# Optimization experiments

Measured on AMD Instinct MI355X. Metric: run time of the kernel, lower is better.

## Reference

```python
import jax, jax.numpy as jnp
import numpy as np

K, P = 20, 20  # neighbors and progressive enlargement step


def _conv1x1(w, x):  # w: (Cout, Cin), x: (B, Cin, N) -> (B, Cout, N)
    return jnp.einsum('oc,bcn->bon', w, x)


def _group_norm(x, gamma, beta, groups, eps=1e-5):  # x: (B, C, N)
    B, C, N = x.shape
    xg = x.reshape(B, groups, C // groups, N)
    m = jnp.mean(xg, axis=(2, 3), keepdims=True)
    v = jnp.var(xg, axis=(2, 3), keepdims=True)
    xn = ((xg - m) * jax.lax.rsqrt(v + eps)).reshape(B, C, N)
    return xn * gamma[None, :, None] + beta[None, :, None]


def _block(x, w, g, b, groups):  # Conv1d(k=1) + GroupNorm + LeakyReLU(0.2)
    h = _group_norm(_conv1x1(w, x), g, b, groups)
    return jnp.where(h > 0, h, 0.2 * h)


def _gather_max(f, idx):  # f: (B, C, N), idx: (B, N, k) -> (B, C, N)
    ft = jnp.swapaxes(f, 1, 2)  # (B, N, C)
    g = jax.vmap(lambda ff, ii: ff[ii])(ft, idx)  # (B, N, k, C)
    return jnp.swapaxes(jnp.max(g, axis=2), 1, 2)


def _forward(x,
             w1a, g1a, b1a, w1b, g1b, b1b,
             w2a, g2a, b2a, w2b, g2b, b2b,
             w3a, g3a, b3a, w3b, g3b, b3b,
             w4a, g4a, b4a, w4b, g4b, b4b,
             w5_1, g5_1, b5_1, w5_2, g5_2, b5_2):
    xc = jnp.swapaxes(x, 1, 2)  # (B, C, N)
    # knn_acc: negative squared pairwise distance, take top-(k+3P)
    xx = jnp.sum(xc * xc, axis=1, keepdims=True)  # (B, 1, N)
    inner = jnp.einsum('bcn,bcm->bnm', xc, xc)  # (B, N, N)
    pd = 2.0 * inner - jnp.swapaxes(xx, 1, 2) - xx  # -||xi-xj||^2
    _, idx_pool = jax.lax.top_k(pd, K + 3 * P)  # (B, N, k+3P)

    def layer(xin, wa, ga, ba, wb, gb, bb, groups, idx):
        fa = _block(xin, wa, ga, ba, groups)
        fb = _block(xin, wb, gb, bb, groups)
        return _gather_max(fa, idx) + fb

    x1 = layer(xc, w1a, g1a, b1a, w1b, g1b, b1b, 8, idx_pool[:, :, :K])
    x2 = layer(x1, w2a, g2a, b2a, w2b, g2b, b2b, 8, idx_pool[:, :, :K + P])
    x3 = layer(x2, w3a, g3a, b3a, w3b, g3b, b3b, 8, idx_pool[:, :, :K + 2 * P])
    x4 = layer(x3, w4a, g4a, b4a, w4b, g4b, b4b, 16, idx_pool)
    x_cat = jnp.concatenate([x1, x2, x3, x4], axis=1)  # (B, 512, N)
    h = _block(x_cat, w5_1, g5_1, b5_1, 16)  # (B, 1024, N)
    h = _block(h, w5_2, g5_2, b5_2, 16)      # (B, 512, N)
    return jnp.swapaxes(h, 1, 2)  # (B, N, 512)


def setup_inputs() -> dict:
    key = jax.random.key(0)
    ks = iter(jax.random.split(key, 16))
    d = {"x": jax.random.normal(next(ks), (8, 2048, 3), dtype=jnp.float32)}

    def add(name, cout, cin):
        d["w" + name] = jax.random.normal(next(ks), (cout, cin), dtype=jnp.float32) * 0.1
        d["g" + name] = jnp.ones((cout,), dtype=jnp.float32)
        d["b" + name] = jnp.zeros((cout,), dtype=jnp.float32)

    add("1a", 64, 3); add("1b", 64, 3)
    add("2a", 64, 64); add("2b", 64, 64)
    add("3a", 128, 64); add("3b", 128, 64)
    add("4a", 256, 128); add("4b", 256, 128)
    add("5_1", 1024, 512); add("5_2", 512, 1024)
    return d


def reference(x,
              w1a, g1a, b1a, w1b, g1b, b1b,
              w2a, g2a, b2a, w2b, g2b, b2b,
              w3a, g3a, b3a, w3b, g3b, b3b,
              w4a, g4a, b4a, w4b, g4b, b4b,
              w5_1, g5_1, b5_1, w5_2, g5_2, b5_2):
    return _forward(x,
                    w1a, g1a, b1a, w1b, g1b, b1b,
                    w2a, g2a, b2a, w2b, g2b, b2b,
                    w3a, g3a, b3a, w3b, g3b, b3b,
                    w4a, g4a, b4a, w4b, g4b, b4b,
                    w5_1, g5_1, b5_1, w5_2, g5_2, b5_2)
```

## Files before the change

kernel.cpp:

```cpp
#include <hip/hip_runtime.h>
#include <stdint.h>

typedef unsigned short u16;
typedef unsigned int u32;
typedef unsigned long long u64;
typedef __attribute__((ext_vector_type(8))) __bf16 bf16x8;
typedef __attribute__((ext_vector_type(8))) u16 u16x8;
typedef __attribute__((ext_vector_type(4))) float f32x4;

#define DEVI __device__ __forceinline__

DEVI u16 f2bf(float f) {
  u32 u = __float_as_uint(f);
  u += 0x7FFFu + ((u >> 16) & 1u);
  return (u16)(u >> 16);
}
DEVI float bf2f(u16 h) { return __uint_as_float(((u32)h) << 16); }
DEVI u16 mono(u16 b) {
  return (b & 0x8000u) ? (u16)~b : (u16)(b | 0x8000u);
}
DEVI u16 unmono(u16 t) {
  return (t & 0x8000u) ? (u16)(t ^ 0x8000u) : (u16)(~t);
}

DEVI void glds16(const void* g, void* l) {
  __builtin_amdgcn_global_load_lds((const __attribute__((address_space(1))) void*)g,
                                   (__attribute__((address_space(3))) void*)l, 16, 0, 0);
}

__global__ void k_pack_all(const float* __restrict__ x, float4* __restrict__ c4,
                           float* __restrict__ gsum,
                           const float* __restrict__ w2a, const float* __restrict__ w2b,
                           const float* __restrict__ w3a, const float* __restrict__ w3b,
                           const float* __restrict__ w4a, const float* __restrict__ w4b,
                           const float* __restrict__ w51, const float* __restrict__ w52,
                           u16* __restrict__ wbf) {
  int g = blockIdx.x * 256 + threadIdx.x;
  if (g < 1792) gsum[g] = 0.f;
  if (g < 16384) {
    float x0 = x[g*3], x1 = x[g*3+1], x2 = x[g*3+2];
    float n = __fadd_rn(__fadd_rn(__fmul_rn(x0,x0), __fmul_rn(x1,x1)), __fmul_rn(x2,x2));
    c4[g] = make_float4(x0, x1, x2, n);
  }
  const float* s; int off;
  if      (g <    4096) { s = w2a; off = g; }
  else if (g <    8192) { s = w2b; off = g - 4096; }
  else if (g <   16384) { s = w3a; off = g - 8192; }
  else if (g <   24576) { s = w3b; off = g - 16384; }
  else if (g <   57344) { s = w4a; off = g - 24576; }
  else if (g <   90112) { s = w4b; off = g - 57344; }
  else if (g <  614400) { s = w51; off = g - 90112; }
  else                  { s = w52; off = g - 614400; }
  wbf[g] = f2bf(s[off]);
}

__global__ __launch_bounds__(256, 8) void k_knn(const float4* __restrict__ c4, int* __restrict__ idxp) {
  __shared__ u64 cand[4][128];
  const int wid = threadIdx.x >> 6;
  const int lane = threadIdx.x & 63;
  const int batch = blockIdx.x & 7;
  const int qib = (blockIdx.x >> 3) * 4 + wid;
  const int blk = (batch << 11) + qib;
  const float4* cb = c4 + (batch << 11);
  const float4 q = cb[qib];

  u32 key[32];
  #pragma unroll
  for (int s = 0; s < 32; ++s) {
    float4 c = cb[s*64 + lane];
    float inner = __fadd_rn(__fadd_rn(__fmul_rn(q.x,c.x), __fmul_rn(q.y,c.y)), __fmul_rn(q.z,c.z));
    float pd = __fsub_rn(__fsub_rn(__fmul_rn(2.0f, inner), q.w), c.w);
    u32 bits = __float_as_uint(pd);
    key[s] = (bits & 0x80000000u) ? ~bits : (bits | 0x80000000u);
  }

  u32 T = 0;
  for (int bit = 30; bit >= 0; --bit) {
    u32 Tc = T | (1u << bit);
    int c = 0;
    #pragma unroll
    for (int s = 0; s < 32; ++s)
      c += __popcll(__ballot(key[s] >= Tc));
    if (c >= 80) { T = Tc; if (c <= 128) break; }
  }

  cand[wid][lane] = 0ull;
  cand[wid][lane + 64] = 0ull;
  asm volatile("s_waitcnt lgkmcnt(0)" ::: "memory");

  const u64 below = (lane == 0) ? 0ull : (~0ull >> (64 - lane));
  int base = 0;
  #pragma unroll
  for (int s = 0; s < 32; ++s) {
    u64 msk = __ballot(key[s] >= T);
    if (key[s] >= T) {
      int pos = base + (int)__popcll(msk & below);
      if (pos < 128)
        cand[wid][pos] = (((u64)key[s]) << 32) | (u32)(2047 - (s*64 + lane));
    }
    base += (int)__popcll(msk);
  }
  asm volatile("s_waitcnt lgkmcnt(0)" ::: "memory");

  u64 v0 = cand[wid][lane];
  u64 v1 = cand[wid][lane + 64];
  #pragma unroll
  for (int k2 = 2; k2 <= 128; k2 <<= 1) {
    #pragma unroll
    for (int j = k2 >> 1; j > 0; j >>= 1) {
      if (j == 64) {
        u64 mx = v0 > v1 ? v0 : v1;
        u64 mn = v0 > v1 ? v1 : v0;
        v0 = mx; v1 = mn;
      } else {
        u64 p0 = __shfl_xor(v0, j, 64);
        u64 p1 = __shfl_xor(v1, j, 64);
        bool lowlane = ((lane & j) == 0);
        bool d0 = ((lane & k2) == 0);
        bool d1 = (((lane + 64) & k2) == 0);
        bool wm0 = (d0 == lowlane);
        bool wm1 = (d1 == lowlane);
        u64 mx0 = v0 > p0 ? v0 : p0, mn0 = v0 > p0 ? p0 : v0;
        u64 mx1 = v1 > p1 ? v1 : p1, mn1 = v1 > p1 ? p1 : v1;
        v0 = wm0 ? mx0 : mn0;
        v1 = wm1 ? mx1 : mn1;
      }
    }
  }

  idxp[(size_t)blk*80 + lane] = 2047 - (int)(u32)v0;
  if (lane < 16) idxp[(size_t)blk*80 + 64 + lane] = 2047 - (int)(u32)v1;
}

__global__ __launch_bounds__(256) void k_conv1(const float* __restrict__ x,
    const float* __restrict__ w1a, const float* __restrict__ w1b,
    const float* __restrict__ g1a, const float* __restrict__ g1b,
    u16* __restrict__ out, float* __restrict__ gsum) {
  __shared__ float xs[384];
  __shared__ float colsum[128], colss[128];
  const int tid = threadIdx.x;
  const int P0 = blockIdx.x * 128;
  for (int i = tid; i < 384; i += 256) xs[i] = x[P0*3 + i];
  if (tid < 128) { colsum[tid] = 0.f; colss[tid] = 0.f; }
  __syncthreads();

  const int c = tid & 127;
  const int half = tid >> 7;
  const float* w = (c < 64) ? (w1a + 3*c) : (w1b + 3*(c-64));
  float wx = w[0], wy = w[1], wz = w[2];
  float gam = (c < 64) ? g1a[c] : g1b[c-64];
  u16 flip = (gam < 0.f) ? (u16)0xFFFF : (u16)0;

  float s = 0.f, ss = 0.f;
  #pragma unroll 4
  for (int p_ = 0; p_ < 64; ++p_) {
    int p = (half << 6) + p_;
    float h = wx*xs[p*3] + wy*xs[p*3+1] + wz*xs[p*3+2];
    s += h; ss += h*h;
    out[(size_t)(P0 + p)*128 + c] = (u16)(mono(f2bf(h)) ^ flip);
  }
  atomicAdd(&colsum[c], s);
  atomicAdd(&colss[c], ss);
  __syncthreads();
  if (tid < 16) {
    float gs = 0.f, gss = 0.f;
    #pragma unroll
    for (int q = 0; q < 8; ++q) { gs += colsum[tid*8+q]; gss += colss[tid*8+q]; }
    int b = blockIdx.x >> 4;
    atomicAdd(&gsum[(b*16 + tid)*2],   gs);
    atomicAdd(&gsum[(b*16 + tid)*2+1], gss);
  }
}

__global__ __launch_bounds__(256) void k_gather(const u16* __restrict__ conv, int Ctot, int Ca,
    int CgShift, int NG, const float* __restrict__ gsum,
    const float* __restrict__ ga, const float* __restrict__ ba,
    const float* __restrict__ gb, const float* __restrict__ bb,
    const int* __restrict__ idxp, int k,
    u16* __restrict__ xcat, int outOff, int lppShift) {
  const int batch = blockIdx.x & 7;
  const int blkin = blockIdx.x >> 3;
  const int lgid = blkin * 256 + threadIdx.x;
  const int p_in = lgid >> lppShift;
  const int c8 = (lgid & ((1 << lppShift) - 1)) * 8;
  const int p = (batch << 11) + p_in;
  const int* irow = idxp + (size_t)p * 80;
  const u16* cb = conv + ((size_t)(batch << 11)) * Ctot + c8;

  const int gia = c8 >> CgShift;
  const int gib = (Ca + c8) >> CgShift;
  const float cnt = (float)(2048 << CgShift);
  float2 sa = *(const float2*)(gsum + (size_t)(batch*NG + gia)*2);
  float2 sb = *(const float2*)(gsum + (size_t)(batch*NG + gib)*2);
  float meanA = sa.x / cnt, rstdA = rsqrtf(sa.y / cnt - meanA*meanA + 1e-5f);
  float meanB = sb.x / cnt, rstdB = rsqrtf(sb.y / cnt - meanB*meanB + 1e-5f);

  float gav[8], bav[8], gbv[8], bbv[8];
  *(float4*)&gav[0] = *(const float4*)(ga + c8); *(float4*)&gav[4] = *(const float4*)(ga + c8 + 4);
  *(float4*)&bav[0] = *(const float4*)(ba + c8); *(float4*)&bav[4] = *(const float4*)(ba + c8 + 4);
  *(float4*)&gbv[0] = *(const float4*)(gb + c8); *(float4*)&gbv[4] = *(const float4*)(gb + c8 + 4);
  *(float4*)&bbv[0] = *(const float4*)(bb + c8); *(float4*)&bbv[4] = *(const float4*)(bb + c8 + 4);

  u16x8 fbv = *(const u16x8*)(conv + (size_t)p * Ctot + Ca + c8);

  u16x8 m8 = (u16x8)(u16)0;
  for (int j0 = 0; j0 < k; j0 += 4) {
    int4 mi4 = *(const int4*)(irow + j0);
    int mis[4] = {mi4.x, mi4.y, mi4.z, mi4.w};
    u16x8 rows[4];
    #pragma unroll
    for (int u = 0; u < 4; ++u)
      rows[u] = *(const u16x8*)(cb + (size_t)mis[u] * Ctot);
    #pragma unroll
    for (int u = 0; u < 4; ++u)
      m8 = __builtin_elementwise_max(m8, rows[u]);
  }

  u16 ov[8];
  #pragma unroll
  for (int q = 0; q < 8; ++q) {
    u16 fA = (gav[q] < 0.f) ? (u16)0xFFFF : (u16)0;
    u16 fB = (gbv[q] < 0.f) ? (u16)0xFFFF : (u16)0;
    float xa = bf2f(unmono((u16)((u16)m8[q] ^ fA)));
    float ha = (xa - meanA) * rstdA * gav[q] + bav[q];
    ha = ha > 0.f ? ha : 0.2f * ha;
    float xb = bf2f(unmono((u16)((u16)fbv[q] ^ fB)));
    float hb = (xb - meanB) * rstdB * gbv[q] + bbv[q];
    hb = hb > 0.f ? hb : 0.2f * hb;
    ov[q] = f2bf(ha + hb);
  }
  *(u16x8*)(xcat + (size_t)p * 512 + outOff + c8) = *(u16x8*)ov;
}

__global__ void k_sb51(const float* __restrict__ gsum, const float* __restrict__ g,
                       const float* __restrict__ b, float* __restrict__ sc,
                       float* __restrict__ bi) {
  int i = blockIdx.x * 256 + threadIdx.x;
  int bb = i >> 10, c = i & 1023;
  int grp = c >> 6;
  float2 s = *(const float2*)(gsum + (size_t)(bb*16 + grp)*2);
  float mean = s.x / 131072.f;
  float rstd = rsqrtf(s.y / 131072.f - mean*mean + 1e-5f);
  float A = rstd * g[c];
  sc[i] = A;
  bi[i] = b[c] - mean * A;
}

__global__ __launch_bounds__(256) void k_apply52(const u16* __restrict__ h2,
    float* __restrict__ outp, const float* __restrict__ gsum,
    const float* __restrict__ g, const float* __restrict__ b) {
  int gid = blockIdx.x * 256 + threadIdx.x;
  size_t e = (size_t)gid * 8;
  int row = (int)(e >> 9);
  int c = (int)e & 511;
  int grp = c >> 5;
  float2 s = *(const float2*)(gsum + (size_t)((row >> 11)*16 + grp)*2);
  const float cnt = 65536.f;
  float mean = s.x / cnt, rstd = rsqrtf(s.y / cnt - mean*mean + 1e-5f);
  u16x8 v = *(const u16x8*)(h2 + e);
  float gv[8], bv[8];
  *(float4*)&gv[0] = *(const float4*)(g + c); *(float4*)&gv[4] = *(const float4*)(g + c + 4);
  *(float4*)&bv[0] = *(const float4*)(b + c); *(float4*)&bv[4] = *(const float4*)(b + c + 4);
  float h[8];
  #pragma unroll
  for (int q = 0; q < 8; ++q) {
    float xv = bf2f((u16)v[q]);
    float o = (xv - mean) * rstd * gv[q] + bv[q];
    h[q] = o > 0.f ? o : 0.2f * o;
  }
  *(float4*)(outp + e)     = make_float4(h[0], h[1], h[2], h[3]);
  *(float4*)(outp + e + 4) = make_float4(h[4], h[5], h[6], h[7]);
}

template<int OUTF32, int MONO, int TRANSA>
__global__ __launch_bounds__(256) void k_gemm(const u16* __restrict__ A, int lda,
    const u16* __restrict__ Bw, int K, void* __restrict__ outp, int ldc,
    int CgShift, int NG, float* __restrict__ gsum,
    const float* __restrict__ ga, const float* __restrict__ gb, int Ca,
    const float* __restrict__ scA, const float* __restrict__ biA) {
  constexpr int BK = 64;
  __shared__ __align__(16) u16 As[128 * BK];
  __shared__ __align__(16) u16 Bs[128 * BK];
  __shared__ float colsum[128], colss[128];
  const int tid = threadIdx.x;
  const int wid = tid >> 6, lane = tid & 63;
  const int tileM = blockIdx.x * 128, tileN = blockIdx.y * 128;
  const int wm = wid >> 1, wn = wid & 1;
  const int lr = lane & 15, lk = (lane >> 4) * 8;
  const float* scb = TRANSA ? (scA + (size_t)(tileM >> 11) * 1024) : nullptr;
  const float* bib = TRANSA ? (biA + (size_t)(tileM >> 11) * 1024) : nullptr;
  f32x4 acc[4][4] = {};
  for (int k0 = 0; k0 < K; k0 += BK) {
    __syncthreads();
    #pragma unroll
    for (int i = 0; i < 4; ++i) {
      int flat = i * 256 + tid;
      int row = flat >> 3, ck = flat & 7;
      if (TRANSA) {
        int cbase = k0 + ck * 8;
        uint4 v = *(const uint4*)(A + (size_t)(tileM + row) * lda + cbase);
        float4 s0 = *(const float4*)(scb + cbase);
        float4 s1 = *(const float4*)(scb + cbase + 4);
        float4 b0 = *(const float4*)(bib + cbase);
        float4 b1 = *(const float4*)(bib + cbase + 4);
        float sc8[8] = {s0.x,s0.y,s0.z,s0.w,s1.x,s1.y,s1.z,s1.w};
        float bi8[8] = {b0.x,b0.y,b0.z,b0.w,b1.x,b1.y,b1.z,b1.w};
        u32 vv[4] = {v.x, v.y, v.z, v.w};
        u32 ov[4];
        #pragma unroll
        for (int q2 = 0; q2 < 4; ++q2) {
          float x0 = bf2f((u16)(vv[q2] & 0xFFFF));
          float x1 = bf2f((u16)(vv[q2] >> 16));
          float o0 = x0 * sc8[q2*2]   + bi8[q2*2];
          float o1 = x1 * sc8[q2*2+1] + bi8[q2*2+1];
          o0 = o0 > 0.f ? o0 : 0.2f * o0;
          o1 = o1 > 0.f ? o1 : 0.2f * o1;
          ov[q2] = (u32)f2bf(o0) | (((u32)f2bf(o1)) << 16);
        }
        *(uint4*)((char*)As + flat * 16) = make_uint4(ov[0], ov[1], ov[2], ov[3]);
      } else {
        glds16(A + (size_t)(tileM + row) * lda + (k0 + ck * 8), (char*)As + flat * 16);
      }
    }
    #pragma unroll
    for (int i = 0; i < 4; ++i) {
      int flat = i * 256 + tid;
      int row = flat >> 3, ck = flat & 7;
      glds16(Bw + (size_t)(tileN + row) * K + (k0 + ck * 8), (char*)Bs + flat * 16);
    }
    __syncthreads();
    #pragma unroll
    for (int ks = 0; ks < 2; ++ks) {
      bf16x8 af[4], bfr[4];
      #pragma unroll
      for (int i = 0; i < 4; ++i)
        af[i] = *(const bf16x8*)&As[(wm*64 + i*16 + lr) * BK + ks*32 + lk];
      #pragma unroll
      for (int j = 0; j < 4; ++j)
        bfr[j] = *(const bf16x8*)&Bs[(wn*64 + j*16 + lr) * BK + ks*32 + lk];
      #pragma unroll
      for (int i = 0; i < 4; ++i)
        #pragma unroll
        for (int j = 0; j < 4; ++j)
          acc[i][j] = __builtin_amdgcn_mfma_f32_16x16x32_bf16(af[i], bfr[j], acc[i][j], 0, 0, 0);
    }
  }
  const int orow0 = tileM + wm*64 + ((lane >> 4) * 4);
  const int ocol0 = tileN + wn*64 + lr;

  u16 flip[4] = {0,0,0,0};
  if (MONO) {
    #pragma unroll
    for (int j = 0; j < 4; ++j) {
      int colg = ocol0 + j*16;
      float gm = (colg < Ca) ? ga[colg] : gb[colg - Ca];
      flip[j] = (gm < 0.f) ? (u16)0xFFFF : (u16)0;
    }
  }

  float csum[4] = {0.f,0.f,0.f,0.f}, css[4] = {0.f,0.f,0.f,0.f};
  #pragma unroll
  for (int i = 0; i < 4; ++i)
    #pragma unroll
    for (int j = 0; j < 4; ++j)
      #pragma unroll
      for (int r = 0; r < 4; ++r) {
        int row = orow0 + i*16 + r;
        int col = ocol0 + j*16;
        float v = acc[i][j][r];
        csum[j] += v; css[j] += v*v;
        if (OUTF32) ((float*)outp)[(size_t)row * ldc + col] = v;
        else {
          u16 st = f2bf(v);
          if (MONO) st = (u16)(mono(st) ^ flip[j]);
          ((u16*)outp)[(size_t)row * ldc + col] = st;
        }
      }

  #pragma unroll
  for (int mask = 16; mask <= 32; mask <<= 1)
    #pragma unroll
    for (int j = 0; j < 4; ++j) {
      csum[j] += __shfl_xor(csum[j], mask, 64);
      css[j]  += __shfl_xor(css[j],  mask, 64);
    }
  if (tid < 128) { colsum[tid] = 0.f; colss[tid] = 0.f; }
  __syncthreads();
  if ((lane >> 4) == 0) {
    #pragma unroll
    for (int j = 0; j < 4; ++j) {
      int col = wn*64 + j*16 + lr;
      atomicAdd(&colsum[col], csum[j]);
      atomicAdd(&colss[col],  css[j]);
    }
  }
  __syncthreads();
  const int NGtile = 128 >> CgShift;
  if (tid < NGtile) {
    float s = 0.f, ss = 0.f;
    const int Cg = 1 << CgShift;
    for (int c0 = tid << CgShift; c0 < (tid << CgShift) + Cg; ++c0) { s += colsum[c0]; ss += colss[c0]; }
    int b = tileM >> 11;
    int gidx = (tileN >> CgShift) + tid;
    atomicAdd(&gsum[(size_t)(b*NG + gidx)*2],   s);
    atomicAdd(&gsum[(size_t)(b*NG + gidx)*2+1], ss);
  }
}

extern "C" void kernel_launch(void* const* d_in, const int* in_sizes, int n_in,
                              void* d_out, int out_size, void* d_ws, size_t ws_size,
                              hipStream_t stream) {
  const float* x   = (const float*)d_in[0];
  const float* w1a = (const float*)d_in[1];
  const float* g1a = (const float*)d_in[2];
  const float* b1a = (const float*)d_in[3];
  const float* w1b = (const float*)d_in[4];
  const float* g1b = (const float*)d_in[5];
  const float* b1b = (const float*)d_in[6];
  const float* w2a = (const float*)d_in[7];
  const float* g2a = (const float*)d_in[8];
  const float* b2a = (const float*)d_in[9];
  const float* w2b = (const float*)d_in[10];
  const float* g2b = (const float*)d_in[11];
  const float* b2b = (const float*)d_in[12];
  const float* w3a = (const float*)d_in[13];
  const float* g3a = (const float*)d_in[14];
  const float* b3a = (const float*)d_in[15];
  const float* w3b = (const float*)d_in[16];
  const float* g3b = (const float*)d_in[17];
  const float* b3b = (const float*)d_in[18];
  const float* w4a = (const float*)d_in[19];
  const float* g4a = (const float*)d_in[20];
  const float* b4a = (const float*)d_in[21];
  const float* w4b = (const float*)d_in[22];
  const float* g4b = (const float*)d_in[23];
  const float* b4b = (const float*)d_in[24];
  const float* w51 = (const float*)d_in[25];
  const float* g51 = (const float*)d_in[26];
  const float* b51 = (const float*)d_in[27];
  const float* w52 = (const float*)d_in[28];
  const float* g52 = (const float*)d_in[29];
  const float* b52 = (const float*)d_in[30];

  char* ws = (char*)d_ws;
  int*    idxp   = (int*)   (ws + 0);
  float4* c4     = (float4*)(ws + 5242880);
  u16*    wbf    = (u16*)   (ws + 5505024);
  float*  gsum   = (float*) (ws + 7782400);
  u16*    convAB = (u16*)   (ws + 7790592);
  u16*    h1     = (u16*)   (ws + 24567808);
  u16*    xcat   = (u16*)   (ws + 58122240);
  float*  sc51   = (float*) (ws + 0);
  float*  bi51   = (float*) (ws + 32768);
  u16*    h2     = (u16*)   (ws + 7790592);
  u16* wc2 = wbf, *wc3 = wbf + 8192, *wc4 = wbf + 24576;
  u16* w51b = wbf + 90112, *w52b = wbf + 614400;
  float* outf = (float*)d_out;
  float* gsL1 = gsum;        float* gsL2 = gsum + 256;  float* gsL3 = gsum + 512;
  float* gsL4 = gsum + 768;  float* gs51 = gsum + 1280; float* gs52 = gsum + 1536;

  k_pack_all<<<4448, 256, 0, stream>>>(x, c4, gsum, w2a, w2b, w3a, w3b, w4a, w4b,
                                       w51, w52, wbf);
  k_knn<<<4096, 256, 0, stream>>>(c4, idxp);

  k_conv1<<<128, 256, 0, stream>>>(x, w1a, w1b, g1a, g1b, convAB, gsL1);
  k_gather<<<512, 256, 0, stream>>>(convAB, 128, 64, 3, 16, gsL1,
                                    g1a, b1a, g1b, b1b, idxp, 20, xcat, 0, 3);

  k_gemm<0,1,0><<<dim3(128,1), 256, 0, stream>>>(xcat + 0, 512, wc2, 64, convAB, 128,
                                                 3, 16, gsL2, g2a, g2b, 64, nullptr, nullptr);
  k_gather<<<512, 256, 0, stream>>>(convAB, 128, 64, 3, 16, gsL2,
                                    g2a, b2a, g2b, b2b, idxp, 40, xcat, 64, 3);

  k_gemm<0,1,0><<<dim3(128,2), 256, 0, stream>>>(xcat + 64, 512, wc3, 64, convAB, 256,
                                                 4, 16, gsL3, g3a, g3b, 128, nullptr, nullptr);
  k_gather<<<1024, 256, 0, stream>>>(convAB, 256, 128, 4, 16, gsL3,
                                     g3a, b3a, g3b, b3b, idxp, 60, xcat, 128, 4);

  k_gemm<0,1,0><<<dim3(128,4), 256, 0, stream>>>(xcat + 128, 512, wc4, 128, convAB, 512,
                                                 4, 32, gsL4, g4a, g4b, 256, nullptr, nullptr);
  k_gather<<<2048, 256, 0, stream>>>(convAB, 512, 256, 4, 32, gsL4,
                                     g4a, b4a, g4b, b4b, idxp, 80, xcat, 256, 5);

  k_gemm<0,0,0><<<dim3(128,8), 256, 0, stream>>>(xcat, 512, w51b, 512, h1, 1024,
                                                 6, 16, gs51, g51, g51, 1024, nullptr, nullptr);
  k_sb51<<<32, 256, 0, stream>>>(gs51, g51, b51, sc51, bi51);

  k_gemm<0,0,1><<<dim3(128,4), 256, 0, stream>>>(h1, 1024, w52b, 1024, h2, 512,
                                                 5, 16, gs52, g52, g52, 512, sc51, bi51);
  k_apply52<<<4096, 256, 0, stream>>>(h2, outf, gs52, g52, b52);
}
```

Measured before the change: 250.1 us.

## Fuse conv1 into kNN launch and skip radix threshold bits using row max

Merges the layer-1 convolution kernel into the kNN kernel as 128 extra blocks, which removes one launch and lets the cheap conv work overlap with kNN. The kNN threshold search now computes the wave-wide maximum key, excluding the self-distance key, and skips radix bits that cannot be set while the threshold is still on that maximum's prefix. This is meant to cut the number of ballot/popcount passes. The trade-off is extra shared memory per block, which may lower occupancy, and more branch logic in the search loop.

```diff
diff --git a/kernel.cpp b/kernel.cpp
--- a/kernel.cpp
+++ b/kernel.cpp
@@ -54,10 +54,54 @@
   wbf[g] = f2bf(s[off]);
 }
 
-__global__ __launch_bounds__(256, 8) void k_knn(const float4* __restrict__ c4, int* __restrict__ idxp) {
+__global__ __launch_bounds__(256, 8) void k_knn_conv1(
+    const float4* __restrict__ c4, int* __restrict__ idxp,
+    const float* __restrict__ x,
+    const float* __restrict__ w1a, const float* __restrict__ w1b,
+    const float* __restrict__ g1a, const float* __restrict__ g1b,
+    u16* __restrict__ convout, float* __restrict__ gsum) {
   __shared__ u64 cand[4][128];
-  const int wid = threadIdx.x >> 6;
-  const int lane = threadIdx.x & 63;
+  __shared__ float xs[384];
+  __shared__ float colsum[128], colss[128];
+  const int tid = threadIdx.x;
+
+  if (blockIdx.x >= 4096) {
+    const int P0 = (blockIdx.x - 4096) * 128;
+    for (int i = tid; i < 384; i += 256) xs[i] = x[P0*3 + i];
+    if (tid < 128) { colsum[tid] = 0.f; colss[tid] = 0.f; }
+    __syncthreads();
+
+    const int c = tid & 127;
+    const int half = tid >> 7;
+    const float* w = (c < 64) ? (w1a + 3*c) : (w1b + 3*(c-64));
+    float wx = w[0], wy = w[1], wz = w[2];
+    float gam = (c < 64) ? g1a[c] : g1b[c-64];
+    u16 flip = (gam < 0.f) ? (u16)0xFFFF : (u16)0;
+
+    float s = 0.f, ss = 0.f;
+    #pragma unroll 4
+    for (int p_ = 0; p_ < 64; ++p_) {
+      int p = (half << 6) + p_;
+      float h = wx*xs[p*3] + wy*xs[p*3+1] + wz*xs[p*3+2];
+      s += h; ss += h*h;
+      convout[(size_t)(P0 + p)*128 + c] = (u16)(mono(f2bf(h)) ^ flip);
+    }
+    atomicAdd(&colsum[c], s);
+    atomicAdd(&colss[c], ss);
+    __syncthreads();
+    if (tid < 16) {
+      float gs = 0.f, gss = 0.f;
+      #pragma unroll
+      for (int q = 0; q < 8; ++q) { gs += colsum[tid*8+q]; gss += colss[tid*8+q]; }
+      int b = P0 >> 11;
+      atomicAdd(&gsum[(b*16 + tid)*2],   gs);
+      atomicAdd(&gsum[(b*16 + tid)*2+1], gss);
+    }
+    return;
+  }
+
+  const int wid = tid >> 6;
+  const int lane = tid & 63;
   const int batch = blockIdx.x & 7;
   const int qib = (blockIdx.x >> 3) * 4 + wid;
   const int blk = (batch << 11) + qib;
@@ -74,14 +118,29 @@
     key[s] = (bits & 0x80000000u) ? ~bits : (bits | 0x80000000u);
   }
 
+  u32 Mh = 0;
+  #pragma unroll
+  for (int s = 0; s < 32; ++s) {
+    u32 kk = key[s];
+    if (kk != 0x80000000u && kk > Mh) Mh = kk;
+  }
+  #pragma unroll
+  for (int m = 32; m; m >>= 1) {
+    u32 o = __shfl_xor(Mh, m, 64);
+    if (o > Mh) Mh = o;
+  }
+
   u32 T = 0;
+  bool onpfx = ((Mh & 0x80000000u) == 0u);
   for (int bit = 30; bit >= 0; --bit) {
+    if (onpfx && !((Mh >> bit) & 1u)) continue;
     u32 Tc = T | (1u << bit);
     int c = 0;
     #pragma unroll
     for (int s = 0; s < 32; ++s)
       c += __popcll(__ballot(key[s] >= Tc));
     if (c >= 80) { T = Tc; if (c <= 128) break; }
+    else onpfx = false;
   }
 
   cand[wid][lane] = 0ull;
@@ -130,46 +189,6 @@
 
   idxp[(size_t)blk*80 + lane] = 2047 - (int)(u32)v0;
   if (lane < 16) idxp[(size_t)blk*80 + 64 + lane] = 2047 - (int)(u32)v1;
-}
-
-__global__ __launch_bounds__(256) void k_conv1(const float* __restrict__ x,
-    const float* __restrict__ w1a, const float* __restrict__ w1b,
-    const float* __restrict__ g1a, const float* __restrict__ g1b,
-    u16* __restrict__ out, float* __restrict__ gsum) {
-  __shared__ float xs[384];
-  __shared__ float colsum[128], colss[128];
-  const int tid = threadIdx.x;
-  const int P0 = blockIdx.x * 128;
-  for (int i = tid; i < 384; i += 256) xs[i] = x[P0*3 + i];
-  if (tid < 128) { colsum[tid] = 0.f; colss[tid] = 0.f; }
-  __syncthreads();
-
-  const int c = tid & 127;
-  const int half = tid >> 7;
-  const float* w = (c < 64) ? (w1a + 3*c) : (w1b + 3*(c-64));
-  float wx = w[0], wy = w[1], wz = w[2];
-  float gam = (c < 64) ? g1a[c] : g1b[c-64];
-  u16 flip = (gam < 0.f) ? (u16)0xFFFF : (u16)0;
-
-  float s = 0.f, ss = 0.f;
-  #pragma unroll 4
-  for (int p_ = 0; p_ < 64; ++p_) {
-    int p = (half << 6) + p_;
-    float h = wx*xs[p*3] + wy*xs[p*3+1] + wz*xs[p*3+2];
-    s += h; ss += h*h;
-    out[(size_t)(P0 + p)*128 + c] = (u16)(mono(f2bf(h)) ^ flip);
-  }
-  atomicAdd(&colsum[c], s);
-  atomicAdd(&colss[c], ss);
-  __syncthreads();
-  if (tid < 16) {
-    float gs = 0.f, gss = 0.f;
-    #pragma unroll
-    for (int q = 0; q < 8; ++q) { gs += colsum[tid*8+q]; gss += colss[tid*8+q]; }
-    int b = blockIdx.x >> 4;
-    atomicAdd(&gsum[(b*16 + tid)*2],   gs);
-    atomicAdd(&gsum[(b*16 + tid)*2+1], gss);
-  }
 }
 
 __global__ __launch_bounds__(256) void k_gather(const u16* __restrict__ conv, int Ctot, int Ca,
@@ -461,9 +480,9 @@
 
   k_pack_all<<<4448, 256, 0, stream>>>(x, c4, gsum, w2a, w2b, w3a, w3b, w4a, w4b,
                                        w51, w52, wbf);
-  k_knn<<<4096, 256, 0, stream>>>(c4, idxp);
-
-  k_conv1<<<128, 256, 0, stream>>>(x, w1a, w1b, g1a, g1b, convAB, gsL1);
+
+  k_knn_conv1<<<4224, 256, 0, stream>>>(c4, idxp, x, w1a, w1b, g1a, g1b, convAB, gsL1);
+
   k_gather<<<512, 256, 0, stream>>>(convAB, 128, 64, 3, 16, gsL1,
                                     g1a, b1a, g1b, b1b, idxp, 20, xcat, 0, 3);
 
```

Result: faster. 244.5 us (-2.2%).
